# Kernel optimization log

Hardware: AMD Instinct MI355X
Metric: run time of the kernel (lower is better)

The kernel has to match this reference:

```python
import jax, jax.numpy as jnp
import numpy as np

NBINS = 256
STRENGTH = 100.0  # __init__ strength kwarg


def _hist_channel(x):
    # x: [N] flattened masked channel -> 256-bin histogram over [min,max]
    lo = jnp.min(x)
    hi = jnp.max(x)
    scale = (NBINS - 1) / jnp.maximum(hi - lo, 1e-12)
    bins = jnp.clip(jnp.floor((x - lo) * scale + 0.5).astype(jnp.int32), 0, NBINS - 1)
    return jnp.zeros((NBINS,), dtype=x.dtype).at[bins].add(1.0)


def _match_channel(x, t_hist):
    # CDF-based histogram matching (cpp.matchHistogram): remap sorted values of x
    # to bin centers of the target histogram; output normalized to [0,1].
    N = x.shape[0]
    idx = jnp.argsort(x)
    t = t_hist * (N / jnp.maximum(jnp.sum(t_hist), 1e-12))
    cdf = jnp.cumsum(t)  # [NBINS]
    ranks = jnp.arange(N, dtype=cdf.dtype) + 0.5
    bins = jnp.clip(jnp.searchsorted(cdf, ranks), 0, NBINS - 1)
    vals = bins.astype(x.dtype) / (NBINS - 1)
    return jnp.zeros_like(x).at[idx].set(vals)


def reference(input, masks, target_hists, target_mins, target_maxs):
    # input: [1,C,H,W]; masks: [S,H,W]; target_hists: [S,C,256]; mins/maxs: [S,C]
    C = input.shape[1]
    x = input[0]  # [C,H,W]

    def per_style(mask, t_hist, t_min, t_max):
        mf = (x * mask[None]).reshape(C, -1)  # masked feature, [C,N]
        hist = jax.vmap(_hist_channel)(mf)    # computed every call (as in source)
        matched = jax.vmap(_match_channel)(mf, t_hist)  # [C,N] in [0,1]
        target = matched * (t_max - t_min)[:, None] + t_min[:, None]
        target = jax.lax.stop_gradient(target)  # torch uses .data (detached)
        loss = 0.01 * STRENGTH * jnp.mean((mf - target) ** 2)  # nn.MSELoss
        return loss, hist

    losses, hists = jax.vmap(per_style)(masks, target_hists, target_mins, target_maxs)
    return jnp.sum(losses), hists


def setup_inputs() -> dict:
    key = jax.random.key(0)
    k1, k2, k3, k4 = jax.random.split(key, 4)
    S, C, H, W = 2, 256, 256, 256
    input = jax.random.normal(k1, (1, C, H, W), dtype=jnp.float32)
    masks = (jax.random.uniform(k2, (S, H, W)) > 0.5).astype(jnp.float32)
    target_hists = jax.random.uniform(k3, (S, C, NBINS), dtype=jnp.float32) * 100.0
    base = jax.random.normal(k4, (S, C), dtype=jnp.float32)
    target_mins = base - 1.0
    target_maxs = base + 1.0
    return {"input": input, "masks": masks, "target_hists": target_hists,
            "target_mins": target_mins, "target_maxs": target_maxs}
```

## Files before the change

### kernel.cpp

```cpp
#include <hip/hip_runtime.h>
#include <math.h>

#define NBINS 256
#define NB    4096
#define PSPL  4

__global__ void mask_bits_kernel(const float* __restrict__ masks,
                                 unsigned* __restrict__ bits, int total)
{
    const int idx = blockIdx.x * blockDim.x + threadIdx.x;
    bool m = false;
    if (idx < total) m = (masks[idx] != 0.0f);
    const unsigned long long b = __ballot(m);
    const int lane = threadIdx.x & 63;
    if (idx < total) {
        if (lane == 0)       bits[idx >> 5] = (unsigned)b;
        else if (lane == 32) bits[idx >> 5] = (unsigned)(b >> 32);
    }
}

__device__ inline void stat4(float4 xv, unsigned w,
                             float& vmin, float& vmax, float& ssq, float& zc)
{
    const float v0 = (w & 1u) ? xv.x : 0.0f;
    const float v1 = (w & 2u) ? xv.y : 0.0f;
    const float v2 = (w & 4u) ? xv.z : 0.0f;
    const float v3 = (w & 8u) ? xv.w : 0.0f;
    vmin = fminf(vmin, fminf(fminf(v0, v1), fminf(v2, v3)));
    vmax = fmaxf(vmax, fmaxf(fmaxf(v0, v1), fmaxf(v2, v3)));
    ssq += v0 * v0 + v1 * v1 + v2 * v2 + v3 * v3;
    zc += (v0 == 0.0f ? 1.0f : 0.0f) + (v1 == 0.0f ? 1.0f : 0.0f)
        + (v2 == 0.0f ? 1.0f : 0.0f) + (v3 == 0.0f ? 1.0f : 0.0f);
}

__global__ __launch_bounds__(256, 4) void stats_kernel(
    const float* __restrict__ x, const unsigned* __restrict__ bits,
    float4* __restrict__ pstats, int C, int N)
{
    const int blk = blockIdx.x;
    const int c = blk / PSPL, p = blk - c * PSPL;
    const float* __restrict__ xc = x + (size_t)c * N;
    const unsigned* __restrict__ wb0 = bits;
    const unsigned* __restrict__ wb1 = bits + (N >> 5);
    const int tid = threadIdx.x, lane = tid & 63, wid = tid >> 6;
    const int seg = N / PSPL;
    const int base = p * seg, end = base + seg;
    __shared__ float wr[8][4];

    float mn0 = 3.4e38f, mx0 = -3.4e38f, sq0 = 0.f, z0 = 0.f;
    float mn1 = 3.4e38f, mx1 = -3.4e38f, sq1 = 0.f, z1 = 0.f;
    const int step = 256 * 4;
    int i = base + tid * 4;
    for (; i + 3 * step < end; i += 4 * step) {
        float4 xv[4]; unsigned w0[4], w1[4];
        #pragma unroll
        for (int q = 0; q < 4; ++q) {
            const int ii = i + q * step;
            xv[q] = *reinterpret_cast<const float4*>(xc + ii);
            w0[q] = wb0[ii >> 5] >> (ii & 31);
            w1[q] = wb1[ii >> 5] >> (ii & 31);
        }
        #pragma unroll
        for (int q = 0; q < 4; ++q) {
            stat4(xv[q], w0[q], mn0, mx0, sq0, z0);
            stat4(xv[q], w1[q], mn1, mx1, sq1, z1);
        }
    }
    for (; i < end; i += step) {
        const float4 xv = *reinterpret_cast<const float4*>(xc + i);
        stat4(xv, wb0[i >> 5] >> (i & 31), mn0, mx0, sq0, z0);
        stat4(xv, wb1[i >> 5] >> (i & 31), mn1, mx1, sq1, z1);
    }
    #pragma unroll
    for (int off = 32; off > 0; off >>= 1) {
        mn0 = fminf(mn0, __shfl_xor(mn0, off));
        mx0 = fmaxf(mx0, __shfl_xor(mx0, off));
        sq0 += __shfl_xor(sq0, off);
        z0  += __shfl_xor(z0, off);
        mn1 = fminf(mn1, __shfl_xor(mn1, off));
        mx1 = fmaxf(mx1, __shfl_xor(mx1, off));
        sq1 += __shfl_xor(sq1, off);
        z1  += __shfl_xor(z1, off);
    }
    if (lane == 0) {
        wr[0][wid] = mn0; wr[1][wid] = mx0; wr[2][wid] = sq0; wr[3][wid] = z0;
        wr[4][wid] = mn1; wr[5][wid] = mx1; wr[6][wid] = sq1; wr[7][wid] = z1;
    }
    __syncthreads();
    if (tid < 2) {
        const int b8 = tid * 4;
        float mn = wr[b8 + 0][0], mx = wr[b8 + 1][0];
        float sq = wr[b8 + 2][0], z = wr[b8 + 3][0];
        for (int k = 1; k < 4; ++k) {
            mn = fminf(mn, wr[b8 + 0][k]); mx = fmaxf(mx, wr[b8 + 1][k]);
            sq += wr[b8 + 2][k]; z += wr[b8 + 3][k];
        }
        pstats[tid * (C * PSPL) + blk] = make_float4(mn, mx, sq, z);
    }
}

__device__ inline void bin4(float4 xv, unsigned w, float lo, float sc16,
                            unsigned* __restrict__ cnt)
{
    const float e[4] = { (w & 1u) ? xv.x : 0.0f, (w & 2u) ? xv.y : 0.0f,
                         (w & 4u) ? xv.z : 0.0f, (w & 8u) ? xv.w : 0.0f };
    #pragma unroll
    for (int j = 0; j < 4; ++j) {
        const float v = e[j];
        if (v != 0.0f) {
            const int jb = min(NB - 1, max(0, (int)floorf((v - lo) * sc16 + 8.0f)));
            atomicAdd(&cnt[jb], 1u);
        }
    }
}

__global__ __launch_bounds__(1024, 4) void match_kernel(
    const float* __restrict__ x, const unsigned* __restrict__ bits,
    const float4* __restrict__ pstats,
    const float* __restrict__ thist, const float* __restrict__ tmins,
    const float* __restrict__ tmaxs,
    float* __restrict__ out, float* __restrict__ lossws, int C, int N)
{
    const int c = blockIdx.x;
    const float* __restrict__ xc = x + (size_t)c * N;
    const unsigned* __restrict__ wb0 = bits;
    const unsigned* __restrict__ wb1 = bits + (N >> 5);
    const int tid = threadIdx.x, lane = tid & 63, wid = tid >> 6;

    __shared__ unsigned cntS[2][2][NB + 1];
    __shared__ float Sarr[2][NBINS];
    __shared__ int   Karr[2][NBINS];
    __shared__ float thsum[2][4];
    __shared__ unsigned ctot[16];
    __shared__ float wtot[16];
    __shared__ float lsum[16];
    __shared__ float stats8[2][4];

    {
        unsigned* cf = &cntS[0][0][0];
        for (int i = tid; i < 2 * 2 * (NB + 1); i += 1024) cf[i] = 0u;
    }
    if (tid < 2) {
        const float4 p0 = pstats[tid * (C * PSPL) + c * PSPL + 0];
        const float4 p1 = pstats[tid * (C * PSPL) + c * PSPL + 1];
        const float4 p2 = pstats[tid * (C * PSPL) + c * PSPL + 2];
        const float4 p3 = pstats[tid * (C * PSPL) + c * PSPL + 3];
        stats8[tid][0] = fminf(fminf(p0.x, p1.x), fminf(p2.x, p3.x));
        stats8[tid][1] = fmaxf(fmaxf(p0.y, p1.y), fmaxf(p2.y, p3.y));
        stats8[tid][2] = (p0.z + p1.z) + (p2.z + p3.z);
        stats8[tid][3] = (p0.w + p1.w) + (p2.w + p3.w);
    }
    const int g  = tid >> 8;
    const int gi = tid & 255;
    const int gw = (tid >> 6) & 3;
    float th = 0.f, thscan = 0.f;
    if (g < 2) {
        th = thist[(size_t)(g * C + c) * NBINS + gi];
        thscan = th;
        #pragma unroll
        for (int off = 1; off < 64; off <<= 1) {
            const float t = __shfl_up(thscan, off);
            if (lane >= off) thscan += t;
        }
        if (lane == 63) thsum[g][gw] = thscan;
    }
    __syncthreads();

    const float lo0 = stats8[0][0], rng0 = fmaxf(stats8[0][1] - lo0, 1e-12f);
    const float lo1 = stats8[1][0], rng1 = fmaxf(stats8[1][1] - lo1, 1e-12f);
    const float sc16_0 = 4080.0f / rng0;
    const float sc16_1 = 4080.0f / rng1;

    if (g < 2) {
        float cross = 0.f, tsum = 0.f;
        #pragma unroll
        for (int w2 = 0; w2 < 4; ++w2) { if (w2 < gw) cross += thsum[g][w2]; tsum += thsum[g][w2]; }
        const float scale = (float)N / fmaxf(tsum, 1e-12f);
        const float cdfv = (thscan + cross) * scale;
        int K = (int)floorf(cdfv - 0.5f) + 1;
        K = min(N, max(0, K));
        if (gi == NBINS - 1) K = N;
        Karr[g][gi] = K;
    }

    const int copy = wid >> 3;
    unsigned* __restrict__ c0 = cntS[0][copy];
    unsigned* __restrict__ c1 = cntS[1][copy];
    const int step = 1024 * 4;
    int i = tid * 4;
    for (; i + 3 * step < N; i += 4 * step) {
        float4 xv[4]; unsigned w0[4], w1[4];
        #pragma unroll
        for (int q = 0; q < 4; ++q) {
            const int ii = i + q * step;
            xv[q] = *reinterpret_cast<const float4*>(xc + ii);
            w0[q] = wb0[ii >> 5] >> (ii & 31);
            w1[q] = wb1[ii >> 5] >> (ii & 31);
        }
        #pragma unroll
        for (int q = 0; q < 4; ++q) {
            bin4(xv[q], w0[q], lo0, sc16_0, c0);
            bin4(xv[q], w1[q], lo1, sc16_1, c1);
        }
    }
    for (; i < N; i += step) {
        const float4 xv = *reinterpret_cast<const float4*>(xc + i);
        bin4(xv, wb0[i >> 5] >> (i & 31), lo0, sc16_0, c0);
        bin4(xv, wb1[i >> 5] >> (i & 31), lo1, sc16_1, c1);
    }
    __syncthreads();

    const int st = tid >> 9;
    const int t  = tid & 511;
    const int b8 = t * 8;
    unsigned c_[8]; float w_[8];
    unsigned csum = 0u; float wsum = 0.f;
    #pragma unroll
    for (int q = 0; q < 8; ++q) {
        c_[q] = cntS[st][0][b8 + q] + cntS[st][1][b8 + q];
        w_[q] = (float)c_[q] * ((float)(b8 + q) - 7.5f);
        csum += c_[q]; wsum += w_[q];
    }
    unsigned cin = csum; float win = wsum;
    #pragma unroll
    for (int off = 1; off < 64; off <<= 1) {
        const unsigned cu = __shfl_up(cin, off);
        const float    wu = __shfl_up(win, off);
        if (lane >= off) { cin += cu; win += wu; }
    }
    if (lane == 63) { ctot[wid] = cin; wtot[wid] = win; }
    __syncthreads();
    unsigned cofs = 0u; float wofs = 0.f;
    #pragma unroll
    for (int w2 = 0; w2 < 16; ++w2)
        if (w2 >= st * 8 && w2 < wid) { cofs += ctot[w2]; wofs += wtot[w2]; }
    unsigned cex = cofs + (cin - csum);
    float    wex = wofs + (win - wsum);
    {
        unsigned* __restrict__ cp = cntS[st][0];
        float*    __restrict__ WF = (float*)cntS[st][1];
        #pragma unroll
        for (int q = 0; q < 8; ++q) {
            cp[b8 + q] = cex; WF[b8 + q] = wex;
            cex += c_[q]; wex += w_[q];
        }
        if (t == 511) { cp[NB] = cex; WF[NB] = wex; }
    }
    __syncthreads();

    if (g < 2) {
        const float lo  = stats8[g][0];
        const float rng = fmaxf(stats8[g][1] - lo, 1e-12f);
        const float sc16 = 4080.0f / rng;
        const float u    = rng / 4080.0f;
        const float schist = 255.0f / rng;
        const unsigned n0 = (unsigned)stats8[g][3];
        const int ib0 = min(NBINS - 1, max(0, (int)floorf((0.0f - lo) * schist + 0.5f)));
        const int b0  = min(NB - 1,    max(0, (int)floorf((0.0f - lo) * sc16 + 8.0f)));
        unsigned* __restrict__ cp = cntS[g][0];
        float*    __restrict__ WF = (float*)cntS[g][1];

        unsigned h = cp[16 * gi + 16] - cp[16 * gi];
        if (gi == ib0) h += n0;
        out[1 + (size_t)(g * C + c) * NBINS + gi] = (float)h;

        const unsigned Z0 = cp[b0];
        const unsigned k = (unsigned)Karr[g][gi];
        float Sv;
        if (gi == NBINS - 1) {
            Sv = lo * (float)cp[NB] + u * WF[NB];
        } else if (k <= Z0) {
            int jlo = 0, jhi = b0;
            while (jlo < jhi) { const int mid = (jlo + jhi + 1) >> 1;
                if (cp[mid] <= k) jlo = mid; else jhi = mid - 1; }
            const unsigned d = k - cp[jlo];
            Sv = lo * (float)k + u * (WF[jlo] + (float)d * ((float)jlo - 7.5f));
        } else if (k <= Z0 + n0) {
            Sv = lo * (float)Z0 + u * WF[b0];
        } else {
            const unsigned k2 = k - n0;
            int jlo = b0, jhi = NB;
            while (jlo < jhi) { const int mid = (jlo + jhi + 1) >> 1;
                if (cp[mid] <= k2) jlo = mid; else jhi = mid - 1; }
            const unsigned d = k2 - cp[jlo];
            Sv = lo * (float)k2 + u * (WF[jlo] + (float)d * ((float)jlo - 7.5f));
        }
        Sarr[g][gi] = Sv;
    }
    __syncthreads();

    float term = 0.f;
    if (g < 2) {
        const float tmn = tmins[g * C + c], tmx = tmaxs[g * C + c];
        const float Tb = ((float)gi / 255.0f) * (tmx - tmn) + tmn;
        const float Sb = Sarr[g][gi];
        const float Sp = (gi == 0) ? 0.f : Sarr[g][gi - 1];
        const int   Kb = Karr[g][gi];
        const int   Kp = (gi == 0) ? 0 : Karr[g][gi - 1];
        term = -2.0f * Tb * (Sb - Sp) + Tb * Tb * (float)(Kb - Kp);
    }
    #pragma unroll
    for (int off = 32; off > 0; off >>= 1) term += __shfl_xor(term, off);
    if (lane == 0) lsum[wid] = term;
    __syncthreads();
    if (tid == 0) {
        const float t0 = (lsum[0] + lsum[1]) + (lsum[2] + lsum[3]);
        const float t1 = (lsum[4] + lsum[5]) + (lsum[6] + lsum[7]);
        const float inv = 1.0f / ((float)C * (float)N);
        lossws[c]     = (stats8[0][2] + t0) * inv;
        lossws[C + c] = (stats8[1][2] + t1) * inv;
    }
}

__global__ void reduce_loss_kernel(const float* __restrict__ lossws,
                                   float* __restrict__ out, int n)
{
    __shared__ float sh[256];
    const int tid = threadIdx.x;
    float v = 0.f;
    for (int i = tid; i < n; i += 256) v += lossws[i];
    sh[tid] = v;
    __syncthreads();
    for (int st = 128; st > 0; st >>= 1) {
        if (tid < st) sh[tid] += sh[tid + st];
        __syncthreads();
    }
    if (tid == 0) out[0] = sh[0];
}

extern "C" void kernel_launch(void* const* d_in, const int* in_sizes, int n_in,
                              void* d_out, int out_size, void* d_ws, size_t ws_size,
                              hipStream_t stream)
{
    const float* x     = (const float*)d_in[0];
    const float* masks = (const float*)d_in[1];
    const float* thist = (const float*)d_in[2];
    const float* tmins = (const float*)d_in[3];
    const float* tmaxs = (const float*)d_in[4];
    float* out = (float*)d_out;

    const int SC = in_sizes[3];
    const long long ratio = (long long)in_sizes[0] / (long long)in_sizes[1];
    const long long csq   = (long long)SC * ratio;
    const int C = (int)(sqrt((double)csq) + 0.5);
    const int S = SC / C;
    const int N = in_sizes[1] / S;
    const int total = in_sizes[1];

    float* lossws = (float*)d_ws;
    const size_t off1 = ((size_t)SC * 4 + 255) & ~(size_t)255;
    float4* pstats = (float4*)((char*)d_ws + off1);
    const size_t off2 = (off1 + (size_t)SC * PSPL * 16 + 255) & ~(size_t)255;
    unsigned* bits = (unsigned*)((char*)d_ws + off2);

    mask_bits_kernel<<<(total + 1023) / 1024, 1024, 0, stream>>>(masks, bits, total);
    stats_kernel<<<C * PSPL, 256, 0, stream>>>(x, bits, pstats, C, N);
    match_kernel<<<C, 1024, 0, stream>>>(x, bits, pstats, thist, tmins, tmaxs,
                                         out, lossws, C, N);
    reduce_loss_kernel<<<1, 256, 0, stream>>>(lossws, out, SC);
}
```

Baseline: 46.63 us.

## Fuse per-channel stats pass into histogram-matching kernel

```diff
diff --git a/kernel.cpp b/kernel.cpp
--- a/kernel.cpp
+++ b/kernel.cpp
@@ -3,7 +3,6 @@
 
 #define NBINS 256
 #define NB    4096
-#define PSPL  4
 
 __global__ void mask_bits_kernel(const float* __restrict__ masks,
                                  unsigned* __restrict__ bits, int total)
@@ -33,25 +32,48 @@
         + (v2 == 0.0f ? 1.0f : 0.0f) + (v3 == 0.0f ? 1.0f : 0.0f);
 }
 
-__global__ __launch_bounds__(256, 4) void stats_kernel(
+__device__ inline void bin4(float4 xv, unsigned w, float lo, float sc16,
+                            unsigned* __restrict__ cnt)
+{
+    const float e[4] = { (w & 1u) ? xv.x : 0.0f, (w & 2u) ? xv.y : 0.0f,
+                         (w & 4u) ? xv.z : 0.0f, (w & 8u) ? xv.w : 0.0f };
+    #pragma unroll
+    for (int j = 0; j < 4; ++j) {
+        const float v = e[j];
+        if (v != 0.0f) {
+            const int jb = min(NB - 1, max(0, (int)floorf((v - lo) * sc16 + 8.0f)));
+            atomicAdd(&cnt[jb], 1u);
+        }
+    }
+}
+
+__global__ __launch_bounds__(1024, 4) void fused_kernel(
     const float* __restrict__ x, const unsigned* __restrict__ bits,
-    float4* __restrict__ pstats, int C, int N)
-{
-    const int blk = blockIdx.x;
-    const int c = blk / PSPL, p = blk - c * PSPL;
+    const float* __restrict__ thist, const float* __restrict__ tmins,
+    const float* __restrict__ tmaxs,
+    float* __restrict__ out, float* __restrict__ lossws, int C, int N)
+{
+    const int c = blockIdx.x;
     const float* __restrict__ xc = x + (size_t)c * N;
     const unsigned* __restrict__ wb0 = bits;
     const unsigned* __restrict__ wb1 = bits + (N >> 5);
     const int tid = threadIdx.x, lane = tid & 63, wid = tid >> 6;
-    const int seg = N / PSPL;
-    const int base = p * seg, end = base + seg;
-    __shared__ float wr[8][4];
+
+    __shared__ unsigned cntS[2][2][NB + 1];
+    __shared__ float Sarr[2][NBINS];
+    __shared__ int   Karr[2][NBINS];
+    __shared__ float thsum[2][4];
+    __shared__ unsigned ctot[16];
+    __shared__ float wtot[16];
+    __shared__ float lsum[16];
+    __shared__ float stats8[2][4];
+    __shared__ float wr[8][16];
 
     float mn0 = 3.4e38f, mx0 = -3.4e38f, sq0 = 0.f, z0 = 0.f;
     float mn1 = 3.4e38f, mx1 = -3.4e38f, sq1 = 0.f, z1 = 0.f;
-    const int step = 256 * 4;
-    int i = base + tid * 4;
-    for (; i + 3 * step < end; i += 4 * step) {
+    const int step = 1024 * 4;
+    int i = tid * 4;
+    for (; i + 3 * step < N; i += 4 * step) {
         float4 xv[4]; unsigned w0[4], w1[4];
         #pragma unroll
         for (int q = 0; q < 4; ++q) {
@@ -66,7 +88,7 @@
             stat4(xv[q], w1[q], mn1, mx1, sq1, z1);
         }
     }
-    for (; i < end; i += step) {
+    for (; i < N; i += step) {
         const float4 xv = *reinterpret_cast<const float4*>(xc + i);
         stat4(xv, wb0[i >> 5] >> (i & 31), mn0, mx0, sq0, z0);
         stat4(xv, wb1[i >> 5] >> (i & 31), mn1, mx1, sq1, z1);
@@ -86,70 +108,7 @@
         wr[0][wid] = mn0; wr[1][wid] = mx0; wr[2][wid] = sq0; wr[3][wid] = z0;
         wr[4][wid] = mn1; wr[5][wid] = mx1; wr[6][wid] = sq1; wr[7][wid] = z1;
     }
-    __syncthreads();
-    if (tid < 2) {
-        const int b8 = tid * 4;
-        float mn = wr[b8 + 0][0], mx = wr[b8 + 1][0];
-        float sq = wr[b8 + 2][0], z = wr[b8 + 3][0];
-        for (int k = 1; k < 4; ++k) {
-            mn = fminf(mn, wr[b8 + 0][k]); mx = fmaxf(mx, wr[b8 + 1][k]);
-            sq += wr[b8 + 2][k]; z += wr[b8 + 3][k];
-        }
-        pstats[tid * (C * PSPL) + blk] = make_float4(mn, mx, sq, z);
-    }
-}
-
-__device__ inline void bin4(float4 xv, unsigned w, float lo, float sc16,
-                            unsigned* __restrict__ cnt)
-{
-    const float e[4] = { (w & 1u) ? xv.x : 0.0f, (w & 2u) ? xv.y : 0.0f,
-                         (w & 4u) ? xv.z : 0.0f, (w & 8u) ? xv.w : 0.0f };
-    #pragma unroll
-    for (int j = 0; j < 4; ++j) {
-        const float v = e[j];
-        if (v != 0.0f) {
-            const int jb = min(NB - 1, max(0, (int)floorf((v - lo) * sc16 + 8.0f)));
-            atomicAdd(&cnt[jb], 1u);
-        }
-    }
-}
-
-__global__ __launch_bounds__(1024, 4) void match_kernel(
-    const float* __restrict__ x, const unsigned* __restrict__ bits,
-    const float4* __restrict__ pstats,
-    const float* __restrict__ thist, const float* __restrict__ tmins,
-    const float* __restrict__ tmaxs,
-    float* __restrict__ out, float* __restrict__ lossws, int C, int N)
-{
-    const int c = blockIdx.x;
-    const float* __restrict__ xc = x + (size_t)c * N;
-    const unsigned* __restrict__ wb0 = bits;
-    const unsigned* __restrict__ wb1 = bits + (N >> 5);
-    const int tid = threadIdx.x, lane = tid & 63, wid = tid >> 6;
-
-    __shared__ unsigned cntS[2][2][NB + 1];
-    __shared__ float Sarr[2][NBINS];
-    __shared__ int   Karr[2][NBINS];
-    __shared__ float thsum[2][4];
-    __shared__ unsigned ctot[16];
-    __shared__ float wtot[16];
-    __shared__ float lsum[16];
-    __shared__ float stats8[2][4];
-
-    {
-        unsigned* cf = &cntS[0][0][0];
-        for (int i = tid; i < 2 * 2 * (NB + 1); i += 1024) cf[i] = 0u;
-    }
-    if (tid < 2) {
-        const float4 p0 = pstats[tid * (C * PSPL) + c * PSPL + 0];
-        const float4 p1 = pstats[tid * (C * PSPL) + c * PSPL + 1];
-        const float4 p2 = pstats[tid * (C * PSPL) + c * PSPL + 2];
-        const float4 p3 = pstats[tid * (C * PSPL) + c * PSPL + 3];
-        stats8[tid][0] = fminf(fminf(p0.x, p1.x), fminf(p2.x, p3.x));
-        stats8[tid][1] = fmaxf(fmaxf(p0.y, p1.y), fmaxf(p2.y, p3.y));
-        stats8[tid][2] = (p0.z + p1.z) + (p2.z + p3.z);
-        stats8[tid][3] = (p0.w + p1.w) + (p2.w + p3.w);
-    }
+
     const int g  = tid >> 8;
     const int gi = tid & 255;
     const int gw = (tid >> 6) & 3;
@@ -164,6 +123,22 @@
         }
         if (lane == 63) thsum[g][gw] = thscan;
     }
+    {
+        unsigned* cf = &cntS[0][0][0];
+        for (int k = tid; k < 2 * 2 * (NB + 1); k += 1024) cf[k] = 0u;
+    }
+    __syncthreads();
+
+    if (tid < 2) {
+        const int b8 = tid * 4;
+        float mn = wr[b8 + 0][0], mx = wr[b8 + 1][0];
+        float sq = wr[b8 + 2][0], z = wr[b8 + 3][0];
+        for (int k = 1; k < 16; ++k) {
+            mn = fminf(mn, wr[b8 + 0][k]); mx = fmaxf(mx, wr[b8 + 1][k]);
+            sq += wr[b8 + 2][k]; z += wr[b8 + 3][k];
+        }
+        stats8[tid][0] = mn; stats8[tid][1] = mx; stats8[tid][2] = sq; stats8[tid][3] = z;
+    }
     __syncthreads();
 
     const float lo0 = stats8[0][0], rng0 = fmaxf(stats8[0][1] - lo0, 1e-12f);
@@ -186,8 +161,7 @@
     const int copy = wid >> 3;
     unsigned* __restrict__ c0 = cntS[0][copy];
     unsigned* __restrict__ c1 = cntS[1][copy];
-    const int step = 1024 * 4;
-    int i = tid * 4;
+    i = tid * 4;
     for (; i + 3 * step < N; i += 4 * step) {
         float4 xv[4]; unsigned w0[4], w1[4];
         #pragma unroll
@@ -349,13 +323,10 @@
 
     float* lossws = (float*)d_ws;
     const size_t off1 = ((size_t)SC * 4 + 255) & ~(size_t)255;
-    float4* pstats = (float4*)((char*)d_ws + off1);
-    const size_t off2 = (off1 + (size_t)SC * PSPL * 16 + 255) & ~(size_t)255;
-    unsigned* bits = (unsigned*)((char*)d_ws + off2);
+    unsigned* bits = (unsigned*)((char*)d_ws + off1);
 
     mask_bits_kernel<<<(total + 1023) / 1024, 1024, 0, stream>>>(masks, bits, total);
-    stats_kernel<<<C * PSPL, 256, 0, stream>>>(x, bits, pstats, C, N);
-    match_kernel<<<C, 1024, 0, stream>>>(x, bits, pstats, thist, tmins, tmaxs,
+    fused_kernel<<<C, 1024, 0, stream>>>(x, bits, thist, tmins, tmaxs,
                                          out, lossws, C, N);
     reduce_loss_kernel<<<1, 256, 0, stream>>>(lossws, out, SC);
 }
```

Result: faster. 43.76 us (-6.2%).
